# Kernel tuning notes

Measured on AMD Instinct MI355X. Metric: run time of the kernel, lower is better.

Reference implementation:

```python
import jax, jax.numpy as jnp
import numpy as np

B, L, T = 256, 256, 50  # batch, max_len, num_tags


def setup_inputs() -> dict:
    key = jax.random.key(0)
    k1, k2, k3 = jax.random.split(key, 3)
    feats = jax.random.normal(k1, (B, L, T), dtype=jnp.float32)
    trans_m = jax.random.normal(k2, (T, T), dtype=jnp.float32)
    tags = jax.random.randint(k3, (B, L), 0, T)
    mask = jnp.ones((B, L), dtype=jnp.int32)
    return {"feats": feats, "trans_m": trans_m, "tags": tags, "mask": mask}


def _normalizer(logits, trans_m, m):
    # logits: (L, B, T), m: (L, B) float mask
    alpha0 = logits[0]  # (B, T)

    def step(alpha, inp):
        emit, mt = inp  # (B, T), (B,)
        # (B, T_from, T_to) broadcast add, logsumexp over T_from
        tmp = alpha[:, :, None] + trans_m[None, :, :] + emit[:, None, :]
        new = jax.nn.logsumexp(tmp, axis=1)
        alpha = jnp.where(mt[:, None] > 0, new, alpha)
        return alpha, None

    alpha, _ = jax.lax.scan(step, alpha0, (logits[1:], m[1:]))
    return jax.nn.logsumexp(alpha, axis=1)  # (B,)


def _gold_score(logits, trans_m, tags_t, m):
    # logits: (L, B, T); tags_t: (L, B); m: (L, B)
    trans_sc = trans_m[tags_t[:-1], tags_t[1:]] * m[1:]  # (L-1, B)
    emit_sc = jnp.take_along_axis(logits, tags_t[:, :, None], axis=2)[..., 0] * m  # (L, B)
    return jnp.sum(trans_sc + emit_sc[:-1], axis=0) + emit_sc[-1]  # (B,)


def reference(feats, trans_m, tags, mask):
    # feats: (B, L, T) -> (L, B, T); include_start_end_trans=False
    logits = jnp.transpose(feats, (1, 0, 2))
    tags_t = tags.T
    m = mask.T.astype(feats.dtype)
    all_path = _normalizer(logits, trans_m, m)
    gold = _gold_score(logits, trans_m, tags_t, m)
    return all_path - gold  # (B,) loss per example
```

## Files before the change

### kernel.cpp

```cpp
#include <hip/hip_runtime.h>
#include <math.h>


#define TAGS 50
#define LEN 256
#define INV_LN2 1.4426950408889634f
#define LN2 0.6931471805599453f
#define CH 10

#if __has_builtin(__builtin_amdgcn_exp2f)
#define EXP2F(x) __builtin_amdgcn_exp2f(x)
#else
#define EXP2F(x) exp2f(x)
#endif
#if __has_builtin(__builtin_amdgcn_logf)
#define LOG2F(x) __builtin_amdgcn_logf(x)
#else
#define LOG2F(x) log2f(x)
#endif

__device__ __forceinline__ float readlane_f(float v, int srclane) {
  return __builtin_bit_cast(float,
      __builtin_amdgcn_readlane(__builtin_bit_cast(int, v), srclane));
}

__global__ __launch_bounds__(64) void crf_fwd_kernel(
    const float* __restrict__ feats,
    const float* __restrict__ trans,
    const int*   __restrict__ tags,
    const int*   __restrict__ mask,
    float*       __restrict__ out)
{
  const int b    = blockIdx.x;
  const int lane = threadIdx.x;
  const int toc  = lane < TAGS ? lane : (TAGS - 1);

  __shared__ __align__(16) float feats_lds[LEN * TAGS];
  __shared__ int mask_lds[LEN];

  const float* fb = feats + (size_t)b * (LEN * TAGS);
  const int*   tb = tags + b * LEN;
  const int*   mb = mask + b * LEN;

  int tg_c[4], tg_p[4];
#pragma unroll
  for (int k = 0; k < 4; ++k) {
    const int p = lane + 64 * k;
    tg_c[k] = tb[p];
    tg_p[k] = (p >= 1) ? tb[p - 1] : 0;
  }

  {
    const float4* fv = (const float4*)fb;
    for (int i = lane; i < (LEN * TAGS) / 4; i += 64) {
      float4 v = fv[i];
      v.x *= INV_LN2; v.y *= INV_LN2; v.z *= INV_LN2; v.w *= INV_LN2;
      *(float4*)&feats_lds[i * 4] = v;
    }
    for (int i = lane; i < LEN; i += 64) mask_lds[i] = mb[i];
  }

  float E2[TAGS];
#pragma unroll
  for (int f = 0; f < TAGS; ++f)
    E2[f] = EXP2F(trans[f * TAGS + toc] * INV_LN2);

  __syncthreads();

  float A = feats_lds[toc];
  float S = 0.0f;

  float e_nxt = feats_lds[TAGS + toc];
  int   m_nxt = mask_lds[1];

  for (int l = 1; l < LEN; ++l) {
    const float e_cur = e_nxt;
    const int   m_cur = m_nxt;
    const int   ln = (l + 1 < LEN) ? (l + 1) : (LEN - 1);
    e_nxt = feats_lds[ln * TAGS + toc];
    m_nxt = mask_lds[ln];

    const float c  = readlane_f(A, 0);
    const float w  = EXP2F(A);
    const float ec = e_cur - c;
    const float Ac = A - c;

    float acc[4] = {0.0f, 0.0f, 0.0f, 0.0f};
    float buf[2][CH];
#pragma unroll
    for (int j = 0; j < CH; ++j) buf[0][j] = readlane_f(w, j);
#pragma unroll
    for (int ch = 0; ch < 5; ++ch) {
      if (ch < 4) {
#pragma unroll
        for (int j = 0; j < CH; ++j)
          buf[(ch + 1) & 1][j] = readlane_f(w, (ch + 1) * CH + j);
      }
#pragma unroll
      for (int j = 0; j < CH; ++j)
        acc[j & 3] = fmaf(buf[ch & 1][j], E2[ch * CH + j], acc[j & 3]);
    }
    const float p = (acc[0] + acc[1]) + (acc[2] + acc[3]);
    const float raw = LOG2F(p) + ec;
    A = (m_cur > 0) ? raw : Ac;
    S += c;
  }

  if (lane >= TAGS) A = -INFINITY;

  float mx = A;
#pragma unroll
  for (int off = 32; off; off >>= 1) mx = fmaxf(mx, __shfl_xor(mx, off, 64));
  float sum = EXP2F(A - mx);
#pragma unroll
  for (int off = 32; off; off >>= 1) sum += __shfl_xor(sum, off, 64);

  float gp = 0.0f;
#pragma unroll
  for (int k = 0; k < 4; ++k) {
    const int p = lane + 64 * k;
    if (mask_lds[p] > 0) {
      float v = feats_lds[p * TAGS + tg_c[k]] * LN2;
      if (p >= 1) v += trans[tg_p[k] * TAGS + tg_c[k]];
      gp += v;
    }
  }
#pragma unroll
  for (int off = 32; off; off >>= 1) gp += __shfl_xor(gp, off, 64);

  if (lane == 0) {
    const float all_path = LN2 * (S + mx + LOG2F(sum));
    out[b] = all_path - gp;
  }
}

extern "C" void kernel_launch(void* const* d_in, const int* in_sizes, int n_in,
                              void* d_out, int out_size, void* d_ws, size_t ws_size,
                              hipStream_t stream) {
  const float* feats = (const float*)d_in[0];
  const float* trans = (const float*)d_in[1];
  const int*   tags  = (const int*)d_in[2];
  const int*   mask  = (const int*)d_in[3];
  float* out = (float*)d_out;

  const int B = out_size;
  crf_fwd_kernel<<<B, 64, 0, stream>>>(feats, trans, tags, mask, out);
}
```

Before: 122.2 us.

## Compute CRF forward recurrence with bf16 MFMA in linear-probability space

Replaces the per-step scalar readlane/FMA loop over 50 source tags with a matrix-vector product done by eight 16x16x32 bf16 MFMA instructions. exp(trans) is packed once into bf16 B fragments, and the state vector is broadcast into A fragments with ds_bpermute. The recurrence now runs in linear space: each step is scaled by lane 0's value, with log2 of that scale added to a running total, instead of doing a log per step. This removes about 50 readlanes and FMAs per step, but bf16 rounding of the probabilities and the transition matrix adds numerical error. It also depends on lane 0's value staying nonzero for the rescaling to be safe.

```diff
diff --git a/kernel.cpp b/kernel.cpp
--- a/kernel.cpp
+++ b/kernel.cpp
@@ -6,7 +6,9 @@
 #define LEN 256
 #define INV_LN2 1.4426950408889634f
 #define LN2 0.6931471805599453f
-#define CH 10
+
+typedef __attribute__((ext_vector_type(8))) short bf16x8;
+typedef __attribute__((ext_vector_type(4))) float f32x4;
 
 #if __has_builtin(__builtin_amdgcn_exp2f)
 #define EXP2F(x) __builtin_amdgcn_exp2f(x)
@@ -18,10 +20,21 @@
 #else
 #define LOG2F(x) log2f(x)
 #endif
+#if __has_builtin(__builtin_amdgcn_rcpf)
+#define RCPF(x) __builtin_amdgcn_rcpf(x)
+#else
+#define RCPF(x) (1.0f / (x))
+#endif
 
 __device__ __forceinline__ float readlane_f(float v, int srclane) {
   return __builtin_bit_cast(float,
       __builtin_amdgcn_readlane(__builtin_bit_cast(int, v), srclane));
+}
+
+__device__ __forceinline__ int bf16pair(float lo, float hi) {
+  unsigned lb = (__builtin_bit_cast(unsigned, lo) + 0x8000u) >> 16;
+  unsigned hb = (__builtin_bit_cast(unsigned, hi) + 0x8000u) & 0xFFFF0000u;
+  return (int)(hb | lb);
 }
 
 __global__ __launch_bounds__(64) void crf_fwd_kernel(
@@ -34,6 +47,8 @@
   const int b    = blockIdx.x;
   const int lane = threadIdx.x;
   const int toc  = lane < TAGS ? lane : (TAGS - 1);
+  const int q    = lane >> 4;
+  const int n    = lane & 15;
 
   __shared__ __align__(16) float feats_lds[LEN * TAGS];
   __shared__ int mask_lds[LEN];
@@ -60,58 +75,85 @@
     for (int i = lane; i < LEN; i += 64) mask_lds[i] = mb[i];
   }
 
-  float E2[TAGS];
+  union U8 { int i[4]; bf16x8 v; };
+  U8 Bfr[4][2];
 #pragma unroll
-  for (int f = 0; f < TAGS; ++f)
-    E2[f] = EXP2F(trans[f * TAGS + toc] * INV_LN2);
+  for (int t = 0; t < 4; ++t)
+#pragma unroll
+    for (int c = 0; c < 2; ++c)
+#pragma unroll
+      for (int r = 0; r < 4; ++r) {
+        const int f0 = 32 * c + 8 * q + 2 * r;
+        const int to = 16 * t + n;
+        const float e0 = (f0 < TAGS && to < TAGS)
+            ? EXP2F(trans[f0 * TAGS + to] * INV_LN2) : 0.0f;
+        const float e1 = (f0 + 1 < TAGS && to < TAGS)
+            ? EXP2F(trans[(f0 + 1) * TAGS + to] * INV_LN2) : 0.0f;
+        Bfr[t][c].i[r] = bf16pair(e0, e1);
+      }
+
+  int addrA[2][4];
+#pragma unroll
+  for (int c = 0; c < 2; ++c)
+#pragma unroll
+    for (int r = 0; r < 4; ++r)
+      addrA[c][r] = (32 * c + 8 * q + 2 * r) * 4;
 
   __syncthreads();
 
-  float A = feats_lds[toc];
-  float S = 0.0f;
+  const float padf = (lane < TAGS) ? 1.0f : 0.0f;
+  const float e0 = feats_lds[toc];
+  const float c0 = readlane_f(e0, 0);
+  float v = EXP2F(e0 - c0) * padf;
+  float S = c0;
 
-  float e_nxt = feats_lds[TAGS + toc];
+  float ehat_nxt = EXP2F(feats_lds[TAGS + toc]) * padf;
   int   m_nxt = mask_lds[1];
 
+  const f32x4 zero4 = {0.0f, 0.0f, 0.0f, 0.0f};
+
   for (int l = 1; l < LEN; ++l) {
-    const float e_cur = e_nxt;
+    const float ehat = ehat_nxt;
     const int   m_cur = m_nxt;
     const int   ln = (l + 1 < LEN) ? (l + 1) : (LEN - 1);
-    e_nxt = feats_lds[ln * TAGS + toc];
+    const float e_raw = feats_lds[ln * TAGS + toc];
     m_nxt = mask_lds[ln];
 
-    const float c  = readlane_f(A, 0);
-    const float w  = EXP2F(A);
-    const float ec = e_cur - c;
-    const float Ac = A - c;
+    const float partner = __shfl_xor(v, 1, 64);
+    const float lo = (lane & 1) ? partner : v;
+    const float hi = (lane & 1) ? v : partner;
+    const int pk = bf16pair(lo, hi);
 
-    float acc[4] = {0.0f, 0.0f, 0.0f, 0.0f};
-    float buf[2][CH];
+    U8 A0, A1;
 #pragma unroll
-    for (int j = 0; j < CH; ++j) buf[0][j] = readlane_f(w, j);
-#pragma unroll
-    for (int ch = 0; ch < 5; ++ch) {
-      if (ch < 4) {
-#pragma unroll
-        for (int j = 0; j < CH; ++j)
-          buf[(ch + 1) & 1][j] = readlane_f(w, (ch + 1) * CH + j);
-      }
-#pragma unroll
-      for (int j = 0; j < CH; ++j)
-        acc[j & 3] = fmaf(buf[ch & 1][j], E2[ch * CH + j], acc[j & 3]);
+    for (int r = 0; r < 4; ++r) {
+      A0.i[r] = __builtin_amdgcn_ds_bpermute(addrA[0][r], pk);
+      A1.i[r] = __builtin_amdgcn_ds_bpermute(addrA[1][r], pk);
     }
-    const float p = (acc[0] + acc[1]) + (acc[2] + acc[3]);
-    const float raw = LOG2F(p) + ec;
-    A = (m_cur > 0) ? raw : Ac;
-    S += c;
+
+    f32x4 d0 = __builtin_amdgcn_mfma_f32_16x16x32_bf16(A0.v, Bfr[0][0].v, zero4, 0, 0, 0);
+    f32x4 d1 = __builtin_amdgcn_mfma_f32_16x16x32_bf16(A0.v, Bfr[1][0].v, zero4, 0, 0, 0);
+    f32x4 d2 = __builtin_amdgcn_mfma_f32_16x16x32_bf16(A0.v, Bfr[2][0].v, zero4, 0, 0, 0);
+    f32x4 d3 = __builtin_amdgcn_mfma_f32_16x16x32_bf16(A0.v, Bfr[3][0].v, zero4, 0, 0, 0);
+    d0 = __builtin_amdgcn_mfma_f32_16x16x32_bf16(A1.v, Bfr[0][1].v, d0, 0, 0, 0);
+    d1 = __builtin_amdgcn_mfma_f32_16x16x32_bf16(A1.v, Bfr[1][1].v, d1, 0, 0, 0);
+    d2 = __builtin_amdgcn_mfma_f32_16x16x32_bf16(A1.v, Bfr[2][1].v, d2, 0, 0, 0);
+    d3 = __builtin_amdgcn_mfma_f32_16x16x32_bf16(A1.v, Bfr[3][1].v, d3, 0, 0, 0);
+
+    const float p01 = (lane & 16) ? d1[0] : d0[0];
+    const float p23 = (lane & 16) ? d3[0] : d2[0];
+    const float d   = (lane & 32) ? p23 : p01;
+
+    const float cand = d * ehat;
+    const float vnew = (m_cur > 0) ? cand : v;
+    const float cc = readlane_f(vnew, 0);
+    const float rr = RCPF(cc);
+    v = vnew * rr;
+    S += LOG2F(cc);
+    ehat_nxt = EXP2F(e_raw) * padf;
   }
 
-  if (lane >= TAGS) A = -INFINITY;
-
-  float mx = A;
-#pragma unroll
-  for (int off = 32; off; off >>= 1) mx = fmaxf(mx, __shfl_xor(mx, off, 64));
-  float sum = EXP2F(A - mx);
+  float sum = v;
 #pragma unroll
   for (int off = 32; off; off >>= 1) sum += __shfl_xor(sum, off, 64);
 
@@ -120,16 +162,16 @@
   for (int k = 0; k < 4; ++k) {
     const int p = lane + 64 * k;
     if (mask_lds[p] > 0) {
-      float v = feats_lds[p * TAGS + tg_c[k]] * LN2;
-      if (p >= 1) v += trans[tg_p[k] * TAGS + tg_c[k]];
-      gp += v;
+      float vv = feats_lds[p * TAGS + tg_c[k]] * LN2;
+      if (p >= 1) vv += trans[tg_p[k] * TAGS + tg_c[k]];
+      gp += vv;
     }
   }
 #pragma unroll
   for (int off = 32; off; off >>= 1) gp += __shfl_xor(gp, off, 64);
 
   if (lane == 0) {
-    const float all_path = LN2 * (S + mx + LOG2F(sum));
+    const float all_path = LN2 * (S + LOG2F(sum));
     out[b] = all_path - gp;
   }
 }
```

After: 126.5 us. +3.5%, slower.

## Split CRF forward scan into parallel chunked matrix products with MFMA combine

Applied to the files above, without the earlier changes.

The sequential 256-step log-sum-exp scan per batch becomes 8 independent chunks of 32 steps. Each chunk computes a 64x64 transfer matrix in the linear (exp) domain using bf16 MFMA with per-step rescaling, and a second kernel chains the 8 matrices per batch with the initial alpha. This exposes far more parallelism (2048 blocks instead of 256) and moves the inner product onto matrix cores. In exchange it adds a workspace round trip, a second launch, bf16 rounding error in the transition weights and states, and overflow or underflow risk when rescaling by a single pivot element.

```diff
diff --git a/kernel.cpp b/kernel.cpp
--- a/kernel.cpp
+++ b/kernel.cpp
@@ -4,9 +4,14 @@
 
 #define TAGS 50
 #define LEN 256
+#define NB 256
+#define NCH 8
+#define CST 32
 #define INV_LN2 1.4426950408889634f
 #define LN2 0.6931471805599453f
-#define CH 10
+
+typedef __attribute__((ext_vector_type(8))) short bf16x8;
+typedef __attribute__((ext_vector_type(4))) float f32x4;
 
 #if __has_builtin(__builtin_amdgcn_exp2f)
 #define EXP2F(x) __builtin_amdgcn_exp2f(x)
@@ -17,6 +22,11 @@
 #define LOG2F(x) __builtin_amdgcn_logf(x)
 #else
 #define LOG2F(x) log2f(x)
+#endif
+#if __has_builtin(__builtin_amdgcn_rcpf)
+#define RCPF(x) __builtin_amdgcn_rcpf(x)
+#else
+#define RCPF(x) (1.0f / (x))
 #endif
 
 __device__ __forceinline__ float readlane_f(float v, int srclane) {
@@ -24,113 +34,190 @@
       __builtin_amdgcn_readlane(__builtin_bit_cast(int, v), srclane));
 }
 
-__global__ __launch_bounds__(64) void crf_fwd_kernel(
+__device__ __forceinline__ int bfpack(float lo, float hi) {
+  unsigned lb = __builtin_bit_cast(unsigned, lo) + 0x8000u;
+  unsigned hb = __builtin_bit_cast(unsigned, hi) + 0x8000u;
+#if __has_builtin(__builtin_amdgcn_perm)
+  return (int)__builtin_amdgcn_perm(hb, lb, 0x07060302u);
+#else
+  return (int)((hb & 0xFFFF0000u) | (lb >> 16));
+#endif
+}
+
+union U8 { int i[4]; bf16x8 v; };
+
+#define WS_SC(b,c) ((((b) * NCH) + (c)) * 4)
+#define WS_T(b,c)  (NB * NCH * 4 + (((b) * NCH) + (c)) * 4096)
+
+__global__ __launch_bounds__(256, 1) void crf_scan_kernel(
+    const float* __restrict__ feats,
+    const float* __restrict__ trans,
+    const int*   __restrict__ mask,
+    float*       __restrict__ ws)
+{
+  const int bid  = blockIdx.x;
+  const int tid  = threadIdx.x;
+  const int w    = tid >> 6;
+  const int lane = tid & 63;
+  const int q    = (tid >> 4) & 3;
+  const int n    = tid & 15;
+  const f32x4 zero4 = {0.0f, 0.0f, 0.0f, 0.0f};
+
+  const int b  = bid >> 3;
+  const int c  = bid & 7;
+  const int l0 = c * CST;
+  const int lstart = (c == 0) ? 1 : 0;
+
+  __shared__ __align__(16) float eh[CST * 52 + 16];
+  __shared__ int ml[CST];
+
+  for (int i = tid; i < CST * 52 + 16; i += 256) eh[i] = 1.0f;
+  __syncthreads();
+
+  const float* fbc = feats + ((size_t)b * LEN + l0) * TAGS;
+  {
+    const float4* fv = (const float4*)fbc;
+    for (int i = tid; i < (CST * TAGS) / 4; i += 256) {
+      const float4 v4 = fv[i];
+      const int g = i * 4;
+#pragma unroll
+      for (int e = 0; e < 4; ++e) {
+        const int gg = g + e;
+        const int row = gg / TAGS;
+        const int col = gg - row * TAGS;
+        const float val = (e == 0) ? v4.x : (e == 1) ? v4.y : (e == 2) ? v4.z : v4.w;
+        eh[row * 52 + col] = EXP2F(val * INV_LN2);
+      }
+    }
+    if (tid < CST) ml[tid] = mask[b * LEN + l0 + tid];
+  }
+
+  U8 Afr[4][2];
+#pragma unroll
+  for (int tm = 0; tm < 4; ++tm)
+#pragma unroll
+    for (int c2 = 0; c2 < 2; ++c2)
+#pragma unroll
+      for (int rr = 0; rr < 4; ++rr) {
+        const int m = 16 * tm + n;
+        const int kr = 32 * c2 + 16 * (rr >> 1) + 4 * q + 2 * (rr & 1);
+        const float e0 = (m < TAGS && kr < TAGS)
+            ? EXP2F(trans[kr * TAGS + m] * INV_LN2) : 0.0f;
+        const float e1 = (m < TAGS && kr + 1 < TAGS)
+            ? EXP2F(trans[(kr + 1) * TAGS + m] * INV_LN2) : 0.0f;
+        Afr[tm][c2].i[rr] = bfpack(e0, e1);
+      }
+
+  __syncthreads();
+
+  f32x4 d[4];
+#pragma unroll
+  for (int tm = 0; tm < 4; ++tm)
+#pragma unroll
+    for (int e = 0; e < 4; ++e)
+      d[tm][e] = (tm == w && (4 * q + e) == n) ? 1.0f : 0.0f;
+
+  float S = 0.0f;
+
+  for (int l = lstart; l < CST; ++l) {
+    if (ml[l] > 0) {
+      float pvt = d[0][0];
+      pvt = (w == 1) ? d[1][0] : pvt;
+      pvt = (w == 2) ? d[2][0] : pvt;
+      pvt = (w == 3) ? d[3][0] : pvt;
+      const float cc = readlane_f(pvt, 0);
+      const float rv = RCPF(cc);
+      const f32x4 rv4 = {rv, rv, rv, rv};
+
+      U8 B0, B1;
+      B0.i[0] = bfpack(d[0][0], d[0][1]);
+      B0.i[1] = bfpack(d[0][2], d[0][3]);
+      B0.i[2] = bfpack(d[1][0], d[1][1]);
+      B0.i[3] = bfpack(d[1][2], d[1][3]);
+      B1.i[0] = bfpack(d[2][0], d[2][1]);
+      B1.i[1] = bfpack(d[2][2], d[2][3]);
+      B1.i[2] = bfpack(d[3][0], d[3][1]);
+      B1.i[3] = bfpack(d[3][2], d[3][3]);
+
+#pragma unroll
+      for (int tm = 0; tm < 4; ++tm) {
+        f32x4 acc = __builtin_amdgcn_mfma_f32_16x16x32_bf16(
+            Afr[tm][0].v, B0.v, zero4, 0, 0, 0);
+        acc = __builtin_amdgcn_mfma_f32_16x16x32_bf16(
+            Afr[tm][1].v, B1.v, acc, 0, 0, 0);
+        const f32x4 er = *(const f32x4*)&eh[l * 52 + 16 * tm + 4 * q];
+        d[tm] = acc * (er * rv4);
+      }
+      S += LOG2F(cc);
+    }
+  }
+
+  float* tw = ws + WS_T(b, c) + (16 * w + n) * 64;
+#pragma unroll
+  for (int tm = 0; tm < 4; ++tm)
+    *(f32x4*)&tw[16 * tm + 4 * q] = d[tm];
+  if (lane == 0) ws[WS_SC(b, c) + w] = S;
+}
+
+__global__ __launch_bounds__(64) void crf_combine_kernel(
     const float* __restrict__ feats,
     const float* __restrict__ trans,
     const int*   __restrict__ tags,
     const int*   __restrict__ mask,
+    const float* __restrict__ ws,
     float*       __restrict__ out)
 {
-  const int b    = blockIdx.x;
+  const int b = blockIdx.x;
   const int lane = threadIdx.x;
-  const int toc  = lane < TAGS ? lane : (TAGS - 1);
-
-  __shared__ __align__(16) float feats_lds[LEN * TAGS];
-  __shared__ int mask_lds[LEN];
+
+  float x = (lane < TAGS)
+      ? EXP2F(feats[(size_t)b * (LEN * TAGS) + lane] * INV_LN2) : 0.0f;
+  float Ssum = 0.0f;
+
+  for (int c = 0; c < NCH; ++c) {
+    const float sw = ws[WS_SC(b, c) + (lane >> 4)];
+    float m1 = fmaxf(sw, __shfl_xor(sw, 16, 64));
+    const float smax = fmaxf(m1, __shfl_xor(m1, 32, 64));
+    x *= EXP2F(sw - smax);
+
+    const float* Tb = ws + WS_T(b, c) + lane;
+    float a0 = 0.0f, a1 = 0.0f, a2 = 0.0f, a3 = 0.0f;
+#pragma unroll
+    for (int i = 0; i < 64; i += 4) {
+      a0 = fmaf(Tb[(i + 0) * 64], readlane_f(x, i + 0), a0);
+      a1 = fmaf(Tb[(i + 1) * 64], readlane_f(x, i + 1), a1);
+      a2 = fmaf(Tb[(i + 2) * 64], readlane_f(x, i + 2), a2);
+      a3 = fmaf(Tb[(i + 3) * 64], readlane_f(x, i + 3), a3);
+    }
+    const float acc = (a0 + a1) + (a2 + a3);
+    const float cc = readlane_f(acc, 0);
+    x = acc * RCPF(cc);
+    Ssum += smax + LOG2F(cc);
+  }
+
+  float s = x;
+#pragma unroll
+  for (int off = 32; off; off >>= 1) s += __shfl_xor(s, off, 64);
 
   const float* fb = feats + (size_t)b * (LEN * TAGS);
   const int*   tb = tags + b * LEN;
   const int*   mb = mask + b * LEN;
-
-  int tg_c[4], tg_p[4];
+  float gp = 0.0f;
 #pragma unroll
   for (int k = 0; k < 4; ++k) {
     const int p = lane + 64 * k;
-    tg_c[k] = tb[p];
-    tg_p[k] = (p >= 1) ? tb[p - 1] : 0;
-  }
-
-  {
-    const float4* fv = (const float4*)fb;
-    for (int i = lane; i < (LEN * TAGS) / 4; i += 64) {
-      float4 v = fv[i];
-      v.x *= INV_LN2; v.y *= INV_LN2; v.z *= INV_LN2; v.w *= INV_LN2;
-      *(float4*)&feats_lds[i * 4] = v;
-    }
-    for (int i = lane; i < LEN; i += 64) mask_lds[i] = mb[i];
-  }
-
-  float E2[TAGS];
-#pragma unroll
-  for (int f = 0; f < TAGS; ++f)
-    E2[f] = EXP2F(trans[f * TAGS + toc] * INV_LN2);
-
-  __syncthreads();
-
-  float A = feats_lds[toc];
-  float S = 0.0f;
-
-  float e_nxt = feats_lds[TAGS + toc];
-  int   m_nxt = mask_lds[1];
-
-  for (int l = 1; l < LEN; ++l) {
-    const float e_cur = e_nxt;
-    const int   m_cur = m_nxt;
-    const int   ln = (l + 1 < LEN) ? (l + 1) : (LEN - 1);
-    e_nxt = feats_lds[ln * TAGS + toc];
-    m_nxt = mask_lds[ln];
-
-    const float c  = readlane_f(A, 0);
-    const float w  = EXP2F(A);
-    const float ec = e_cur - c;
-    const float Ac = A - c;
-
-    float acc[4] = {0.0f, 0.0f, 0.0f, 0.0f};
-    float buf[2][CH];
-#pragma unroll
-    for (int j = 0; j < CH; ++j) buf[0][j] = readlane_f(w, j);
-#pragma unroll
-    for (int ch = 0; ch < 5; ++ch) {
-      if (ch < 4) {
-#pragma unroll
-        for (int j = 0; j < CH; ++j)
-          buf[(ch + 1) & 1][j] = readlane_f(w, (ch + 1) * CH + j);
-      }
-#pragma unroll
-      for (int j = 0; j < CH; ++j)
-        acc[j & 3] = fmaf(buf[ch & 1][j], E2[ch * CH + j], acc[j & 3]);
-    }
-    const float p = (acc[0] + acc[1]) + (acc[2] + acc[3]);
-    const float raw = LOG2F(p) + ec;
-    A = (m_cur > 0) ? raw : Ac;
-    S += c;
-  }
-
-  if (lane >= TAGS) A = -INFINITY;
-
-  float mx = A;
-#pragma unroll
-  for (int off = 32; off; off >>= 1) mx = fmaxf(mx, __shfl_xor(mx, off, 64));
-  float sum = EXP2F(A - mx);
-#pragma unroll
-  for (int off = 32; off; off >>= 1) sum += __shfl_xor(sum, off, 64);
-
-  float gp = 0.0f;
-#pragma unroll
-  for (int k = 0; k < 4; ++k) {
-    const int p = lane + 64 * k;
-    if (mask_lds[p] > 0) {
-      float v = feats_lds[p * TAGS + tg_c[k]] * LN2;
-      if (p >= 1) v += trans[tg_p[k] * TAGS + tg_c[k]];
-      gp += v;
+    const int tg = tb[p];
+    if (mb[p] > 0) {
+      float vv = fb[p * TAGS + tg];
+      if (p >= 1) vv += trans[tb[p - 1] * TAGS + tg];
+      gp += vv;
     }
   }
 #pragma unroll
   for (int off = 32; off; off >>= 1) gp += __shfl_xor(gp, off, 64);
 
   if (lane == 0) {
-    const float all_path = LN2 * (S + mx + LOG2F(sum));
-    out[b] = all_path - gp;
+    out[b] = LN2 * (Ssum + LOG2F(s)) - gp;
   }
 }
 
@@ -142,7 +229,8 @@
   const int*   tags  = (const int*)d_in[2];
   const int*   mask  = (const int*)d_in[3];
   float* out = (float*)d_out;
-
-  const int B = out_size;
-  crf_fwd_kernel<<<B, 64, 0, stream>>>(feats, trans, tags, mask, out);
-}
+  float* ws  = (float*)d_ws;
+
+  crf_scan_kernel<<<NB * NCH, 256, 0, stream>>>(feats, trans, mask, ws);
+  crf_combine_kernel<<<NB, 64, 0, stream>>>(feats, trans, tags, mask, ws, out);
+}
```

Result: no change. 124.5 us (+1.9%).
